# Optimization experiments

Measured on AMD Instinct MI355X. Metric: run time of the kernel, lower is better.

The kernel has to match this reference:

```python
import jax, jax.numpy as jnp
import numpy as np

TREE = 128
BASIC = 128
EPS = 1e-5


def layer_norm(x, g, b):
    m = jnp.mean(x, axis=-1, keepdims=True)
    v = jnp.mean((x - m) ** 2, axis=-1, keepdims=True)
    return (x - m) * jax.lax.rsqrt(v + EPS) * g + b


def setup_inputs() -> dict:
    key = jax.random.key(0)
    ks = jax.random.split(key, 32)
    n2, n1, n0 = 320000, 80000, 20000
    inp = {
        'subtree_h_top': jax.random.normal(ks[0], (n2, TREE), jnp.float32),
        'atom_x_1': jax.random.normal(ks[1], (n1, BASIC), jnp.float32),
        'atom_x_0': jax.random.normal(ks[2], (n0, BASIC), jnp.float32),
        'bond_x_2': jax.random.normal(ks[3], (n2, BASIC), jnp.float32),
        'bond_x_1': jax.random.normal(ks[4], (n1, BASIC), jnp.float32),
        'branch_W1': jax.random.normal(ks[5], (2, TREE + BASIC, TREE), jnp.float32) * 0.05,
        'branch_b1': jnp.zeros((2, TREE), jnp.float32),
        'branch_g1': jnp.ones((2, TREE), jnp.float32),
        'branch_beta1': jnp.zeros((2, TREE), jnp.float32),
        'branch_W2': jax.random.normal(ks[6], (2, TREE, TREE), jnp.float32) * 0.05,
        'branch_b2': jnp.zeros((2, TREE), jnp.float32),
        'branch_g2': jnp.ones((2, TREE), jnp.float32),
        'branch_beta2': jnp.zeros((2, TREE), jnp.float32),
        'sub_W1': jax.random.normal(ks[7], (2, BASIC + TREE, TREE), jnp.float32) * 0.05,
        'sub_b1': jnp.zeros((2, TREE), jnp.float32),
        'sub_g1': jnp.ones((2, TREE), jnp.float32),
        'sub_beta1': jnp.zeros((2, TREE), jnp.float32),
        'sub_W2': jax.random.normal(ks[8], (2, TREE, TREE), jnp.float32) * 0.05,
        'sub_b2': jnp.zeros((2, TREE), jnp.float32),
        'sub_g2': jnp.ones((2, TREE), jnp.float32),
        'sub_beta2': jnp.zeros((2, TREE), jnp.float32),
        'head_W': jax.random.normal(ks[9], (2, BASIC + TREE, TREE), jnp.float32) * 0.05,
        'head_b': jnp.zeros((2, TREE), jnp.float32),
        'head_g': jnp.ones((2, TREE), jnp.float32),
        'head_beta': jnp.zeros((2, TREE), jnp.float32),
        'src_2': jax.random.randint(ks[10], (n2,), 0, n2),
        'dst_2': jax.random.randint(ks[11], (n2,), 0, n1),
        'src_1': jax.random.randint(ks[12], (n1,), 0, n1),
        'dst_1': jax.random.randint(ks[13], (n1,), 0, n0),
    }
    return inp


def reference(subtree_h_top, atom_x_1, atom_x_0, bond_x_2, bond_x_1,
              branch_W1, branch_b1, branch_g1, branch_beta1,
              branch_W2, branch_b2, branch_g2, branch_beta2,
              sub_W1, sub_b1, sub_g1, sub_beta1,
              sub_W2, sub_b2, sub_g2, sub_beta2,
              head_W, head_b, head_g, head_beta,
              src_2, dst_2, src_1, dst_1):
    relu = jax.nn.relu
    h = subtree_h_top  # subtree_h of level tree_level nodes
    atom_xs = (atom_x_1, atom_x_0)
    bond_xs = (bond_x_2, bond_x_1)
    srcs = (src_2, src_1)
    dsts = (dst_2, dst_1)
    for i in range(2):  # i=0 -> k=2, i=1 -> k=1 (fixed small loop over tree levels)
        ax = atom_xs[i]
        # Branch_Update: edge MLP on [subtree_h[src], bond_x]
        ex = jnp.concatenate([h[srcs[i]], bond_xs[i]], axis=-1)  # [E, tree+basic]
        bh = relu(layer_norm(ex @ branch_W1[i] + branch_b1[i], branch_g1[i], branch_beta1[i]))
        bh = relu(layer_norm(bh @ branch_W2[i] + branch_b2[i], branch_g2[i], branch_beta2[i]))
        # fn.sum aggregation per destination (head) node
        agg = jax.ops.segment_sum(bh, dsts[i], num_segments=ax.shape[0])
        # Tree_Update_Sep
        sx = jnp.concatenate([ax, agg], axis=-1)  # [N, basic+tree]
        f = relu(layer_norm(sx @ sub_W1[i] + sub_b1[i], sub_g1[i], sub_beta1[i]))
        f = relu(layer_norm(f @ sub_W2[i] + sub_b2[i], sub_g2[i], sub_beta2[i]))
        th = jnp.concatenate([ax, f], axis=-1)
        h = relu(layer_norm(th @ head_W[i] + head_b[i], head_g[i], head_beta[i]))
    return h  # subtree_h of atom_0 nodes: [n0, tree_dim]
```

## Files before the change

kernel.cpp:

```cpp
#include <hip/hip_runtime.h>


#define D    128
#define TE   64
#define XS   264
#define TE2  32
#define MAXT 40

typedef float  f32x4 __attribute__((ext_vector_type(4)));
typedef _Float16 f16x8 __attribute__((ext_vector_type(8)));

__device__ __forceinline__ unsigned short f2h(float f) {
    union { _Float16 h; unsigned short u; } x;
    x.h = (_Float16)f;
    return x.u;
}

__global__ __launch_bounds__(256) void pack_zero(
    const float* __restrict__ brW1, const float* __restrict__ brW2,
    const float* __restrict__ sW1,  const float* __restrict__ sW2,
    const float* __restrict__ hW,   unsigned short* __restrict__ Wp,
    int* __restrict__ cnt, int AN)
{
    int p = blockIdx.x * 256 + threadIdx.x;
    if (p < AN) cnt[p] = 0;
    const float* src; int off, K;
    if (p < 65536)       { src = brW1; off = 0;      K = 256; }
    else if (p < 98304)  { src = brW2; off = 65536;  K = 128; }
    else if (p < 163840) { src = sW1;  off = 98304;  K = 256; }
    else if (p < 196608) { src = sW2;  off = 163840; K = 128; }
    else                 { src = hW;   off = 196608; K = 256; }
    int q = p - off, lvl, r;
    if (K == 256) { lvl = q >> 15; r = q & 32767; }
    else          { lvl = q >> 14; r = q & 16383; }
    int kb = r >> 12, n = (r >> 5) & 127, kk = r & 31;
    Wp[p] = f2h(src[(size_t)lvl * K * 128 + (size_t)(kb * 32 + kk) * 128 + n]);
}


__global__ __launch_bounds__(256) void csr_hist(
    const int* __restrict__ dA, int EA, const int* __restrict__ dB, int EB,
    int* __restrict__ cnt, int AOFFv)
{
    int i = blockIdx.x * 256 + threadIdx.x;
    if (i < EA)               atomicAdd(cnt + dA[i], 1);
    else if (i - EA < EB)     atomicAdd(cnt + AOFFv + dB[i - EA], 1);
}

__global__ __launch_bounds__(256) void csr_scanA(
    const int* __restrict__ cnt, int* __restrict__ inc, int* __restrict__ bsum,
    int nbA, int AOFFv)
{
    __shared__ int lds[256];
    int b = blockIdx.x, t = threadIdx.x;
    int lb, ebase, bs;
    if (b < nbA) { lb = b;       ebase = 0;     bs = lb; }
    else         { lb = b - nbA; ebase = AOFFv; bs = 128 + lb; }
    int idx = ebase + lb * 1024 + t * 4;
    int s0 = cnt[idx], s1 = cnt[idx + 1], s2 = cnt[idx + 2], s3 = cnt[idx + 3];
    int p1 = s0 + s1, p2 = p1 + s2, p3 = p2 + s3;
    lds[t] = p3; __syncthreads();
#pragma unroll
    for (int o = 1; o < 256; o <<= 1) {
        int v = (t >= o) ? lds[t - o] : 0;
        __syncthreads();
        lds[t] += v;
        __syncthreads();
    }
    int ex = lds[t] - p3;
    inc[idx] = ex + s0; inc[idx + 1] = ex + p1; inc[idx + 2] = ex + p2; inc[idx + 3] = ex + p3;
    if (t == 255) bsum[bs] = lds[255];
}

__global__ __launch_bounds__(256) void csr_scanC2(
    const int* __restrict__ cnt, int* __restrict__ inc, const int* __restrict__ bsum,
    int* __restrict__ cursor, int nbA, int nbB, int AOFFv)
{
    __shared__ int lds[256];
    int b = blockIdx.x, t = threadIdx.x;
    int seg = t >> 7, i = t & 127;
    int n = seg ? nbB : nbA;
    lds[t] = (i < n) ? bsum[t] : 0;
    __syncthreads();
#pragma unroll
    for (int o = 1; o < 128; o <<= 1) {
        int v = (i >= o) ? lds[t - o] : 0;
        __syncthreads();
        lds[t] += v;
        __syncthreads();
    }
    int lb, ebase, bs;
    if (b < nbA) { lb = b;       ebase = 0;     bs = lb; }
    else         { lb = b - nbA; ebase = AOFFv; bs = 128 + lb; }
    int carry = (lb > 0) ? lds[bs - 1] : 0;
    int idx = ebase + lb * 1024 + t * 4;
#pragma unroll
    for (int j = 0; j < 4; ++j) {
        int v = inc[idx + j] + carry;
        inc[idx + j] = v;
        cursor[idx + j] = v - cnt[idx + j];
    }
}

__global__ __launch_bounds__(256) void csr_pos(
    const int* __restrict__ dA, int EA, const int* __restrict__ dB, int EB,
    int* __restrict__ cursor, int* __restrict__ posA, int* __restrict__ posB, int AOFFv)
{
    int i = blockIdx.x * 256 + threadIdx.x;
    if (i < EA)           posA[i] = atomicAdd(cursor + dA[i], 1);
    else if (i - EA < EB) posB[i - EA] = atomicAdd(cursor + AOFFv + dB[i - EA], 1);
}


__device__ __forceinline__ void ln_relu32(f32x4 acc[4],
    const float* __restrict__ b, const float* __restrict__ g, const float* __restrict__ be,
    float* s_red, float* s_ms, int rb, int cb, int n15, int q, int wcol, int t)
{
#pragma unroll
    for (int ct = 0; ct < 4; ++ct) {
        float bb = b[cb + ct * 16 + n15];
#pragma unroll
        for (int r = 0; r < 4; ++r) acc[ct][r] += bb;
    }
    float sum[4], ss[4];
#pragma unroll
    for (int r = 0; r < 4; ++r) {
        sum[r] = acc[0][r] + acc[1][r] + acc[2][r] + acc[3][r];
        ss[r]  = acc[0][r]*acc[0][r] + acc[1][r]*acc[1][r]
               + acc[2][r]*acc[2][r] + acc[3][r]*acc[3][r];
    }
#pragma unroll
    for (int off = 1; off < 16; off <<= 1) {
#pragma unroll
        for (int r = 0; r < 4; ++r) {
            sum[r] += __shfl_xor(sum[r], off, 64);
            ss[r]  += __shfl_xor(ss[r],  off, 64);
        }
    }
    if (n15 == 0) {
#pragma unroll
        for (int r = 0; r < 4; ++r) {
            int row = rb + q * 4 + r;
            s_red[row * 4 + wcol * 2 + 0] = sum[r];
            s_red[row * 4 + wcol * 2 + 1] = ss[r];
        }
    }
    __syncthreads();
    if (t < TE2) {
        float sm = s_red[t * 4 + 0] + s_red[t * 4 + 2];
        float sq = s_red[t * 4 + 1] + s_red[t * 4 + 3];
        float mean = sm * (1.f / 128.f);
        float var  = sq * (1.f / 128.f) - mean * mean;
        s_ms[t * 2 + 0] = mean;
        s_ms[t * 2 + 1] = rsqrtf(var + 1e-5f);
    }
    __syncthreads();
#pragma unroll
    for (int ct = 0; ct < 4; ++ct) {
        float gg = g[cb + ct * 16 + n15], bb = be[cb + ct * 16 + n15];
#pragma unroll
        for (int r = 0; r < 4; ++r) {
            int row = rb + q * 4 + r;
            float v = (acc[ct][r] - s_ms[row * 2 + 0]) * s_ms[row * 2 + 1] * gg + bb;
            acc[ct][r] = fmaxf(v, 0.f);
        }
    }
}

template<bool HBF16>
__global__ __launch_bounds__(256, 1) void edge_async(
    const void* __restrict__ hsrc, const float* __restrict__ bond,
    const int* __restrict__ src, const int* __restrict__ dstpos,
    const unsigned short* __restrict__ Wp1g, const unsigned short* __restrict__ Wp2g,
    const float* __restrict__ b1, const float* __restrict__ g1, const float* __restrict__ be1,
    const float* __restrict__ b2, const float* __restrict__ g2, const float* __restrict__ be2,
    unsigned short* __restrict__ ebh, int E, int ntiles, int chunk)
{
    __shared__ unsigned short s_w1[32768];
    __shared__ unsigned short s_w2[16384];
    __shared__ unsigned short s_x[2][8192];
    __shared__ int   s_meta[MAXT * 64];
    __shared__ float s_red[TE2 * 4];
    __shared__ float s_ms[TE2 * 2];

    int t = threadIdx.x;
    int tile0 = blockIdx.x * chunk;
    int myT = ntiles - tile0;
    if (myT > chunk) myT = chunk;

    {
        const uint4* w1 = (const uint4*)Wp1g;
        for (int u = t; u < 4096; u += 256) {
            int kb = u >> 9, l = u & 511, n = l >> 2;
            *(uint4*)((char*)s_w1 + kb * 8192 + ((l ^ ((n >> 1) & 3)) << 4)) = w1[u];
        }
        const uint4* w2 = (const uint4*)Wp2g;
        for (int u = t; u < 2048; u += 256) {
            int kb = u >> 9, l = u & 511, n = l >> 2;
            *(uint4*)((char*)s_w2 + kb * 8192 + ((l ^ ((n >> 1) & 3)) << 4)) = w2[u];
        }
        for (int x = t; x < myT * 64; x += 256) {
            int ti = x >> 6, r = x & 63;
            int ge = (tile0 + ti) * TE2 + (r & 31);
            int v;
            if (r < 32) v = (ge < E) ? src[ge] : 0;
            else        v = (ge < E) ? dstpos[ge] : -1;
            s_meta[x] = v;
        }
    }
    __syncthreads();
    if (myT <= 0) return;

    int r0  = t >> 5, k4 = t & 31;
    int r0h = t >> 4, k8 = t & 15;

    {
        if (HBF16) {
            const unsigned short* hp = (const unsigned short*)hsrc;
#pragma unroll
            for (int j = 0; j < 2; ++j) {
                int row = r0h + 16 * j;
                int sv = s_meta[row];
                uint4 v = *(const uint4*)(hp + (size_t)sv * 128 + k8 * 8);
                *(uint4*)((char*)&s_x[0][0] + row * 512 + ((k8 ^ (row & 7)) << 4)) = v;
            }
        } else {
            const float* hp = (const float*)hsrc;
#pragma unroll
            for (int j = 0; j < 4; ++j) {
                int row = r0 + 8 * j;
                int sv = s_meta[row];
                float4 v = *(const float4*)(hp + (size_t)sv * 128 + k4 * 4);
                ushort4 o; o.x = f2h(v.x); o.y = f2h(v.y); o.z = f2h(v.z); o.w = f2h(v.w);
                *(ushort4*)((char*)&s_x[0][0] + row * 512
                            + (((k4 >> 1) ^ (row & 7)) << 4) + (k4 & 1) * 8) = o;
            }
        }
#pragma unroll
        for (int j = 0; j < 4; ++j) {
            int row = r0 + 8 * j;
            int ge = tile0 * TE2 + row;
            float4 v = make_float4(0, 0, 0, 0);
            if (ge < E) v = *(const float4*)(bond + (size_t)ge * 128 + k4 * 4);
            ushort4 o; o.x = f2h(v.x); o.y = f2h(v.y); o.z = f2h(v.z); o.w = f2h(v.w);
            *(ushort4*)((char*)&s_x[0][0] + row * 512
                        + (((16 + (k4 >> 1)) ^ (row & 7)) << 4) + (k4 & 1) * 8) = o;
        }
    }
    __syncthreads();

    int lane = t & 63, w = t >> 6;
    int n15 = lane & 15, q = lane >> 4;
    int rb = (w & 1) * 16, cb = (w >> 1) * 64, wcol = w >> 1;

    int c = 0;
    for (int i = 0; i < myT; ++i) {
        bool hasN = (i + 1 < myT);
        uint4  nh16[2]; float4 nh32[4]; float4 nb[4];
        if (hasN) {
            int mt = i + 1, tb = (tile0 + mt) * TE2;
            if (HBF16) {
                const unsigned short* hp = (const unsigned short*)hsrc;
#pragma unroll
                for (int j = 0; j < 2; ++j) {
                    int row = r0h + 16 * j;
                    int sv = s_meta[mt * 64 + row];
                    nh16[j] = *(const uint4*)(hp + (size_t)sv * 128 + k8 * 8);
                }
            } else {
                const float* hp = (const float*)hsrc;
#pragma unroll
                for (int j = 0; j < 4; ++j) {
                    int row = r0 + 8 * j;
                    int sv = s_meta[mt * 64 + row];
                    nh32[j] = *(const float4*)(hp + (size_t)sv * 128 + k4 * 4);
                }
            }
#pragma unroll
            for (int j = 0; j < 4; ++j) {
                int row = r0 + 8 * j, ge = tb + row;
                nb[j] = make_float4(0, 0, 0, 0);
                if (ge < E) nb[j] = *(const float4*)(bond + (size_t)ge * 128 + k4 * 4);
            }
        }

        const unsigned short* xb = &s_x[c][0];
        unsigned short* f1b = (unsigned short*)&s_x[c ^ 1][0];
        unsigned short* f2b = f1b + 4096;

        f32x4 acc[4];
        f32x4 zero = {0.f, 0.f, 0.f, 0.f};
#pragma unroll
        for (int ct = 0; ct < 4; ++ct) acc[ct] = zero;
#pragma unroll
        for (int kb = 0; kb < 8; ++kb) {
            f16x8 af = *(const f16x8*)((const char*)xb + (rb + n15) * 512
                                       + (((kb * 4 + q) ^ (n15 & 7)) << 4));
#pragma unroll
            for (int ct = 0; ct < 4; ++ct) {
                int n = cb + ct * 16 + n15, l = n * 4 + q;
                f16x8 bf = *(const f16x8*)((const char*)s_w1 + kb * 8192
                                           + ((l ^ ((n >> 1) & 3)) << 4));
                acc[ct] = __builtin_amdgcn_mfma_f32_16x16x32_f16(af, bf, acc[ct], 0, 0, 0);
            }
        }
        ln_relu32(acc, b1, g1, be1, s_red, s_ms, rb, cb, n15, q, wcol, t);
#pragma unroll
        for (int ct = 0; ct < 4; ++ct)
#pragma unroll
            for (int r = 0; r < 4; ++r) {
                int row = rb + q * 4 + r, col = cb + ct * 16 + n15;
                *(unsigned short*)((char*)f1b + row * 256
                                   + ((col * 2) ^ ((row & 7) << 4))) = f2h(acc[ct][r]);
            }
        __syncthreads();

#pragma unroll
        for (int ct = 0; ct < 4; ++ct) acc[ct] = zero;
#pragma unroll
        for (int kb = 0; kb < 4; ++kb) {
            f16x8 af = *(const f16x8*)((const char*)f1b + (rb + n15) * 256
                                       + (((kb * 4 + q) ^ (n15 & 7)) << 4));
#pragma unroll
            for (int ct = 0; ct < 4; ++ct) {
                int n = cb + ct * 16 + n15, l = n * 4 + q;
                f16x8 bf = *(const f16x8*)((const char*)s_w2 + kb * 8192
                                           + ((l ^ ((n >> 1) & 3)) << 4));
                acc[ct] = __builtin_amdgcn_mfma_f32_16x16x32_f16(af, bf, acc[ct], 0, 0, 0);
            }
        }
        ln_relu32(acc, b2, g2, be2, s_red, s_ms, rb, cb, n15, q, wcol, t);
#pragma unroll
        for (int ct = 0; ct < 4; ++ct)
#pragma unroll
            for (int r = 0; r < 4; ++r) {
                int row = rb + q * 4 + r, col = cb + ct * 16 + n15;
                *(unsigned short*)((char*)f2b + row * 256
                                   + ((col * 2) ^ ((row & 7) << 4))) = f2h(acc[ct][r]);
            }
        __syncthreads();

#pragma unroll
        for (int j = 0; j < 2; ++j) {
            int row = r0h + 16 * j;
            int p = s_meta[i * 64 + 32 + row];
            if (p >= 0) {
                uint4 v = *(const uint4*)((const char*)f2b + row * 256
                                          + ((k8 ^ (row & 7)) << 4));
                *(uint4*)(ebh + (size_t)p * 128 + k8 * 8) = v;
            }
        }
        __syncthreads();

        if (hasN) {
            unsigned short* dstb = (unsigned short*)&s_x[c ^ 1][0];
            if (HBF16) {
#pragma unroll
                for (int j = 0; j < 2; ++j) {
                    int row = r0h + 16 * j;
                    *(uint4*)((char*)dstb + row * 512 + ((k8 ^ (row & 7)) << 4)) = nh16[j];
                }
            } else {
#pragma unroll
                for (int j = 0; j < 4; ++j) {
                    int row = r0 + 8 * j;
                    ushort4 o;
                    o.x = f2h(nh32[j].x); o.y = f2h(nh32[j].y);
                    o.z = f2h(nh32[j].z); o.w = f2h(nh32[j].w);
                    *(ushort4*)((char*)dstb + row * 512
                                + (((k4 >> 1) ^ (row & 7)) << 4) + (k4 & 1) * 8) = o;
                }
            }
#pragma unroll
            for (int j = 0; j < 4; ++j) {
                int row = r0 + 8 * j;
                ushort4 o;
                o.x = f2h(nb[j].x); o.y = f2h(nb[j].y); o.z = f2h(nb[j].z); o.w = f2h(nb[j].w);
                *(ushort4*)((char*)dstb + row * 512
                            + (((16 + (k4 >> 1)) ^ (row & 7)) << 4) + (k4 & 1) * 8) = o;
            }
        }
        __syncthreads();
        c ^= 1;
    }
}


template<int KB>
__device__ __forceinline__ void gemm_f16(const unsigned short* s_in, int stride,
    const unsigned short* __restrict__ Wp, int rb, int cb, int n15, int q, f32x4 acc[2][4])
{
    f32x4 zero = {0.f, 0.f, 0.f, 0.f};
#pragma unroll
    for (int m = 0; m < 2; ++m)
#pragma unroll
        for (int ct = 0; ct < 4; ++ct) acc[m][ct] = zero;
#pragma unroll
    for (int kb = 0; kb < KB; ++kb) {
        f16x8 af0 = *(const f16x8*)(s_in + (rb + n15) * stride + kb * 32 + q * 8);
        f16x8 af1 = *(const f16x8*)(s_in + (rb + 16 + n15) * stride + kb * 32 + q * 8);
        const unsigned short* wb = Wp + (size_t)kb * 4096 + q * 8;
#pragma unroll
        for (int ct = 0; ct < 4; ++ct) {
            f16x8 bf = *(const f16x8*)(wb + (cb + ct * 16 + n15) * 32);
            acc[0][ct] = __builtin_amdgcn_mfma_f32_16x16x32_f16(af0, bf, acc[0][ct], 0, 0, 0);
            acc[1][ct] = __builtin_amdgcn_mfma_f32_16x16x32_f16(af1, bf, acc[1][ct], 0, 0, 0);
        }
    }
}

__device__ __forceinline__ void ln_relu(f32x4 acc[2][4],
    const float* __restrict__ b, const float* __restrict__ g, const float* __restrict__ be,
    float* s_red, float* s_ms, int rb, int cb, int n15, int q, int wcol, int t)
{
#pragma unroll
    for (int ct = 0; ct < 4; ++ct) {
        float bb = b[cb + ct * 16 + n15];
#pragma unroll
        for (int m = 0; m < 2; ++m)
#pragma unroll
            for (int r = 0; r < 4; ++r) acc[m][ct][r] += bb;
    }
    float sum[2][4], ss[2][4];
#pragma unroll
    for (int m = 0; m < 2; ++m)
#pragma unroll
        for (int r = 0; r < 4; ++r) {
            sum[m][r] = acc[m][0][r] + acc[m][1][r] + acc[m][2][r] + acc[m][3][r];
            ss[m][r]  = acc[m][0][r]*acc[m][0][r] + acc[m][1][r]*acc[m][1][r]
                      + acc[m][2][r]*acc[m][2][r] + acc[m][3][r]*acc[m][3][r];
        }
#pragma unroll
    for (int off = 1; off < 16; off <<= 1) {
#pragma unroll
        for (int m = 0; m < 2; ++m)
#pragma unroll
            for (int r = 0; r < 4; ++r) {
                sum[m][r] += __shfl_xor(sum[m][r], off, 64);
                ss[m][r]  += __shfl_xor(ss[m][r],  off, 64);
            }
    }
    if (n15 == 0) {
#pragma unroll
        for (int m = 0; m < 2; ++m)
#pragma unroll
            for (int r = 0; r < 4; ++r) {
                int row = rb + m * 16 + q * 4 + r;
                s_red[row * 4 + wcol * 2 + 0] = sum[m][r];
                s_red[row * 4 + wcol * 2 + 1] = ss[m][r];
            }
    }
    __syncthreads();
    if (t < TE) {
        float sm = s_red[t * 4 + 0] + s_red[t * 4 + 2];
        float sq = s_red[t * 4 + 1] + s_red[t * 4 + 3];
        float mean = sm * (1.f / 128.f);
        float var  = sq * (1.f / 128.f) - mean * mean;
        s_ms[t * 2 + 0] = mean;
        s_ms[t * 2 + 1] = rsqrtf(var + 1e-5f);
    }
    __syncthreads();
#pragma unroll
    for (int ct = 0; ct < 4; ++ct) {
        float gg = g[cb + ct * 16 + n15], bb = be[cb + ct * 16 + n15];
#pragma unroll
        for (int m = 0; m < 2; ++m)
#pragma unroll
            for (int r = 0; r < 4; ++r) {
                int row = rb + m * 16 + q * 4 + r;
                float v = (acc[m][ct][r] - s_ms[row * 2 + 0]) * s_ms[row * 2 + 1] * gg + bb;
                acc[m][ct][r] = fmaxf(v, 0.f);
            }
    }
}

template<bool HBF16, bool CSR>
__global__ __launch_bounds__(256, 4) void edge_mlp(
    const void* __restrict__ hsrc, const float* __restrict__ bond,
    const int* __restrict__ src, const int* __restrict__ dstpos,
    const unsigned short* __restrict__ Wp1, const unsigned short* __restrict__ Wp2,
    const float* __restrict__ b1, const float* __restrict__ g1, const float* __restrict__ be1,
    const float* __restrict__ b2, const float* __restrict__ g2, const float* __restrict__ be2,
    float* __restrict__ agg, unsigned short* __restrict__ ebh, int E)
{
    __shared__ unsigned short s_x[TE * XS];
    __shared__ float s_red[TE * 4];
    __shared__ float s_ms[TE * 2];
    __shared__ int s_src[TE], s_idx[TE];
    unsigned short* s_y = s_x + 128;

    int t = threadIdx.x, eb = blockIdx.x * TE;
    if (t < TE) {
        int ge = eb + t;
        s_src[t] = (ge < E) ? src[ge] : -1;
        s_idx[t] = (ge < E) ? dstpos[ge] : -1;
    }
    __syncthreads();

    if (HBF16) {
        const unsigned short* hp = (const unsigned short*)hsrc;
        for (int c = t; c < TE * 16; c += 256) {
            int row = c >> 4, k8 = c & 15;
            int s = s_src[row];
            uint4 v = make_uint4(0, 0, 0, 0);
            if (s >= 0) v = *(const uint4*)(hp + (size_t)s * 128 + k8 * 8);
            *(uint4*)(s_x + row * XS + k8 * 8) = v;
        }
    } else {
        const float* hp = (const float*)hsrc;
        for (int c = t; c < TE * 32; c += 256) {
            int row = c >> 5, k4 = c & 31;
            int s = s_src[row];
            float4 v = make_float4(0, 0, 0, 0);
            if (s >= 0) v = *(const float4*)(hp + (size_t)s * 128 + k4 * 4);
            ushort4 o; o.x = f2h(v.x); o.y = f2h(v.y); o.z = f2h(v.z); o.w = f2h(v.w);
            *(ushort4*)(s_x + row * XS + k4 * 4) = o;
        }
    }
    for (int c = t; c < TE * 32; c += 256) {
        int row = c >> 5, k4 = c & 31;
        int ge = eb + row;
        float4 v = make_float4(0, 0, 0, 0);
        if (ge < E) v = *(const float4*)(bond + (size_t)ge * 128 + k4 * 4);
        ushort4 o; o.x = f2h(v.x); o.y = f2h(v.y); o.z = f2h(v.z); o.w = f2h(v.w);
        *(ushort4*)(s_x + row * XS + 128 + k4 * 4) = o;
    }
    __syncthreads();

    int l = t & 63, w = t >> 6;
    int n15 = l & 15, q = l >> 4;
    int rb = (w & 1) * 32, cb = (w >> 1) * 64, wcol = w >> 1;

    f32x4 acc[2][4];
    gemm_f16<8>(s_x, XS, Wp1, rb, cb, n15, q, acc);
    ln_relu(acc, b1, g1, be1, s_red, s_ms, rb, cb, n15, q, wcol, t);
#pragma unroll
    for (int m = 0; m < 2; ++m)
#pragma unroll
        for (int ct = 0; ct < 4; ++ct)
#pragma unroll
            for (int r = 0; r < 4; ++r)
                s_y[(rb + m * 16 + q * 4 + r) * XS + cb + ct * 16 + n15] = f2h(acc[m][ct][r]);
    __syncthreads();
    gemm_f16<4>(s_y, XS, Wp2, rb, cb, n15, q, acc);
    ln_relu(acc, b2, g2, be2, s_red, s_ms, rb, cb, n15, q, wcol, t);

    if (CSR) {
#pragma unroll
        for (int m = 0; m < 2; ++m)
#pragma unroll
            for (int ct = 0; ct < 4; ++ct)
#pragma unroll
                for (int r = 0; r < 4; ++r)
                    s_x[(rb + m * 16 + q * 4 + r) * XS + cb + ct * 16 + n15] = f2h(acc[m][ct][r]);
        __syncthreads();
        for (int c = t; c < TE * 16; c += 256) {
            int row = c >> 4, k8 = c & 15;
            int p = s_idx[row];
            if (p >= 0)
                *(uint4*)(ebh + (size_t)p * 128 + k8 * 8) =
                    *(const uint4*)(s_x + row * XS + k8 * 8);
        }
    } else {
#pragma unroll
        for (int m = 0; m < 2; ++m)
#pragma unroll
            for (int ct = 0; ct < 4; ++ct)
#pragma unroll
                for (int r = 0; r < 4; ++r) {
                    int row = rb + m * 16 + q * 4 + r;
                    int gd = s_idx[row];
                    if (gd >= 0)
                        atomicAdd(agg + (size_t)gd * D + cb + ct * 16 + n15, acc[m][ct][r]);
                }
    }
}

template<bool OUT_F16, bool CSR>
__global__ __launch_bounds__(256, 4) void node_mlp(
    const float* __restrict__ ax, const float* __restrict__ agg,
    const int* __restrict__ inc, const unsigned short* __restrict__ ebh,
    const unsigned short* __restrict__ Wp1, const unsigned short* __restrict__ Wp2,
    const unsigned short* __restrict__ Wp3,
    const float* __restrict__ b1, const float* __restrict__ g1, const float* __restrict__ be1,
    const float* __restrict__ b2, const float* __restrict__ g2, const float* __restrict__ be2,
    const float* __restrict__ b3, const float* __restrict__ g3, const float* __restrict__ be3,
    void* __restrict__ out, int N)
{
    __shared__ unsigned short s_x[TE * XS];
    __shared__ float s_red[TE * 4];
    __shared__ float s_ms[TE * 2];
    __shared__ int s_beg[TE], s_end[TE];
    unsigned short* s_y = s_x + 128;

    int t = threadIdx.x, nb = blockIdx.x * TE;

    if (CSR && t < TE) {
        int gr = nb + t, b0 = 0, e0 = 0;
        if (gr < N) { e0 = inc[gr]; b0 = (gr == 0) ? 0 : inc[gr - 1]; }
        s_beg[t] = b0; s_end[t] = e0;
    }

    for (int c = t; c < TE * 32; c += 256) {
        int row = c >> 5, k4 = c & 31;
        int gr = nb + row;
        float4 v = make_float4(0, 0, 0, 0);
        if (gr < N) v = *(const float4*)(ax + (size_t)gr * 128 + k4 * 4);
        ushort4 o; o.x = f2h(v.x); o.y = f2h(v.y); o.z = f2h(v.z); o.w = f2h(v.w);
        *(ushort4*)(s_x + row * XS + k4 * 4) = o;
    }

    if (CSR) {
        __syncthreads();
        int r = t >> 2, s4 = t & 3;
        float a[32];
#pragma unroll
        for (int k = 0; k < 32; ++k) a[k] = 0.f;
        int jb = s_beg[r], je = s_end[r];
        int j = jb;
        for (; j + 2 <= je; j += 2) {
            const unsigned short* rp0 = ebh + (size_t)j * 128 + s4 * 32;
            const unsigned short* rp1 = rp0 + 128;
            f16x8 a0 = *(const f16x8*)rp0;
            f16x8 a1 = *(const f16x8*)(rp0 + 8);
            f16x8 a2 = *(const f16x8*)(rp0 + 16);
            f16x8 a3 = *(const f16x8*)(rp0 + 24);
            f16x8 b0 = *(const f16x8*)rp1;
            f16x8 b1v = *(const f16x8*)(rp1 + 8);
            f16x8 b2v = *(const f16x8*)(rp1 + 16);
            f16x8 b3v = *(const f16x8*)(rp1 + 24);
#pragma unroll
            for (int k = 0; k < 8; ++k) {
                a[k]      += (float)a0[k];
                a[8 + k]  += (float)a1[k];
                a[16 + k] += (float)a2[k];
                a[24 + k] += (float)a3[k];
            }
#pragma unroll
            for (int k = 0; k < 8; ++k) {
                a[k]      += (float)b0[k];
                a[8 + k]  += (float)b1v[k];
                a[16 + k] += (float)b2v[k];
                a[24 + k] += (float)b3v[k];
            }
        }
        if (j < je) {
            const unsigned short* rp = ebh + (size_t)j * 128 + s4 * 32;
            f16x8 v0 = *(const f16x8*)rp;
            f16x8 v1 = *(const f16x8*)(rp + 8);
            f16x8 v2 = *(const f16x8*)(rp + 16);
            f16x8 v3 = *(const f16x8*)(rp + 24);
#pragma unroll
            for (int k = 0; k < 8; ++k) {
                a[k]      += (float)v0[k];
                a[8 + k]  += (float)v1[k];
                a[16 + k] += (float)v2[k];
                a[24 + k] += (float)v3[k];
            }
        }
        unsigned short* op = s_x + r * XS + 128 + s4 * 32;
#pragma unroll
        for (int blk = 0; blk < 4; ++blk) {
            f16x8 h;
#pragma unroll
            for (int k = 0; k < 8; ++k) h[k] = (_Float16)a[blk * 8 + k];
            *(f16x8*)(op + blk * 8) = h;
        }
    } else {
        for (int c = t; c < TE * 32; c += 256) {
            int row = c >> 5, k4 = c & 31;
            int gr = nb + row;
            float4 v = make_float4(0, 0, 0, 0);
            if (gr < N) v = *(const float4*)(agg + (size_t)gr * 128 + k4 * 4);
            ushort4 o; o.x = f2h(v.x); o.y = f2h(v.y); o.z = f2h(v.z); o.w = f2h(v.w);
            *(ushort4*)(s_x + row * XS + 128 + k4 * 4) = o;
        }
    }
    __syncthreads();

    int l = t & 63, w = t >> 6;
    int n15 = l & 15, q = l >> 4;
    int rb = (w & 1) * 32, cb = (w >> 1) * 64, wcol = w >> 1;

    f32x4 acc[2][4];
    gemm_f16<8>(s_x, XS, Wp1, rb, cb, n15, q, acc);
    ln_relu(acc, b1, g1, be1, s_red, s_ms, rb, cb, n15, q, wcol, t);
#pragma unroll
    for (int m = 0; m < 2; ++m)
#pragma unroll
        for (int ct = 0; ct < 4; ++ct)
#pragma unroll
            for (int r = 0; r < 4; ++r)
                s_y[(rb + m * 16 + q * 4 + r) * XS + cb + ct * 16 + n15] = f2h(acc[m][ct][r]);
    __syncthreads();
    gemm_f16<4>(s_y, XS, Wp2, rb, cb, n15, q, acc);
    ln_relu(acc, b2, g2, be2, s_red, s_ms, rb, cb, n15, q, wcol, t);
#pragma unroll
    for (int m = 0; m < 2; ++m)
#pragma unroll
        for (int ct = 0; ct < 4; ++ct)
#pragma unroll
            for (int r = 0; r < 4; ++r)
                s_x[(rb + m * 16 + q * 4 + r) * XS + 128 + cb + ct * 16 + n15] = f2h(acc[m][ct][r]);
    __syncthreads();
    gemm_f16<8>(s_x, XS, Wp3, rb, cb, n15, q, acc);
    ln_relu(acc, b3, g3, be3, s_red, s_ms, rb, cb, n15, q, wcol, t);

#pragma unroll
    for (int m = 0; m < 2; ++m)
#pragma unroll
        for (int ct = 0; ct < 4; ++ct)
#pragma unroll
            for (int r = 0; r < 4; ++r) {
                int row = rb + m * 16 + q * 4 + r;
                int gr = nb + row;
                int col = cb + ct * 16 + n15;
                if (gr < N) {
                    if (OUT_F16)
                        ((unsigned short*)out)[(size_t)gr * D + col] = f2h(acc[m][ct][r]);
                    else
                        ((float*)out)[(size_t)gr * D + col] = acc[m][ct][r];
                }
            }
}

extern "C" void kernel_launch(void* const* d_in, const int* in_sizes, int n_in,
                              void* d_out, int out_size, void* d_ws, size_t ws_size,
                              hipStream_t stream)
{
    const float* h2   = (const float*)d_in[0];
    const float* ax1  = (const float*)d_in[1];
    const float* ax0  = (const float*)d_in[2];
    const float* bx2  = (const float*)d_in[3];
    const float* bx1  = (const float*)d_in[4];
    const float* brW1 = (const float*)d_in[5];
    const float* brb1 = (const float*)d_in[6];
    const float* brg1 = (const float*)d_in[7];
    const float* brbe1= (const float*)d_in[8];
    const float* brW2 = (const float*)d_in[9];
    const float* brb2 = (const float*)d_in[10];
    const float* brg2 = (const float*)d_in[11];
    const float* brbe2= (const float*)d_in[12];
    const float* sW1  = (const float*)d_in[13];
    const float* sb1  = (const float*)d_in[14];
    const float* sg1  = (const float*)d_in[15];
    const float* sbe1 = (const float*)d_in[16];
    const float* sW2  = (const float*)d_in[17];
    const float* sb2  = (const float*)d_in[18];
    const float* sg2  = (const float*)d_in[19];
    const float* sbe2 = (const float*)d_in[20];
    const float* hW   = (const float*)d_in[21];
    const float* hb   = (const float*)d_in[22];
    const float* hg   = (const float*)d_in[23];
    const float* hbe  = (const float*)d_in[24];
    const int*   src2 = (const int*)d_in[25];
    const int*   dst2 = (const int*)d_in[26];
    const int*   src1 = (const int*)d_in[27];
    const int*   dst1 = (const int*)d_in[28];

    int n2 = in_sizes[0] / D;
    int n1 = in_sizes[1] / D;
    int n0 = in_sizes[2] / D;

    unsigned short* Wp = (unsigned short*)d_ws;

    const unsigned short* pBr1[2] = { Wp + 0,      Wp + 32768 };
    const unsigned short* pBr2[2] = { Wp + 65536,  Wp + 65536  + 16384 };
    const unsigned short* pS1 [2] = { Wp + 98304,  Wp + 98304  + 32768 };
    const unsigned short* pS2 [2] = { Wp + 163840, Wp + 163840 + 16384 };
    const unsigned short* pH  [2] = { Wp + 196608, Wp + 196608 + 32768 };

    int nbA = (n1 + 1023) / 1024, nbB = (n0 + 1023) / 1024;
    int AOFFv = nbA * 1024;
    int AN = AOFFv + nbB * 1024;
    auto al = [](size_t x) { return (x + 255) & ~(size_t)255; };
    size_t o = 524288;
    size_t cnt_o  = o; o = al(o + (size_t)AN * 4);
    size_t inc_o  = o; o = al(o + (size_t)AN * 4);
    size_t cur_o  = o; o = al(o + (size_t)AN * 4);
    size_t bsum_o = o; o = al(o + 1024);
    size_t posA_o = o; o = al(o + (size_t)n2 * 4);
    size_t posB_o = o; o = al(o + (size_t)n1 * 4);
    size_t h1_o   = o; o = al(o + (size_t)n1 * 256);
    size_t ebh_o  = o; o = al(o + (size_t)n2 * 256);
    size_t o_csr  = o;
    bool use_csr = (nbA <= 128) && (nbB <= 128) && (ws_size >= o_csr);

    int t2e = (n2 + TE - 1) / TE, t1e = (n1 + TE - 1) / TE;
    int t1n = (n1 + TE - 1) / TE, t0n = (n0 + TE - 1) / TE;

    if (use_csr) {
        int*            cnt    = (int*)((char*)d_ws + cnt_o);
        int*            inc    = (int*)((char*)d_ws + inc_o);
        int*            cursor = (int*)((char*)d_ws + cur_o);
        int*            bsum   = (int*)((char*)d_ws + bsum_o);
        int*            posA   = (int*)((char*)d_ws + posA_o);
        int*            posB   = (int*)((char*)d_ws + posB_o);
        unsigned short* h1     = (unsigned short*)((char*)d_ws + h1_o);
        unsigned short* ebh    = (unsigned short*)((char*)d_ws + ebh_o);

        int EG = (n2 + n1 + 255) / 256;
        pack_zero<<<dim3(1024), dim3(256), 0, stream>>>(brW1, brW2, sW1, sW2, hW, Wp, cnt, AN);
        csr_hist  <<<dim3(EG),        dim3(256), 0, stream>>>(dst2, n2, dst1, n1, cnt, AOFFv);
        csr_scanA <<<dim3(nbA + nbB), dim3(256), 0, stream>>>(cnt, inc, bsum, nbA, AOFFv);
        csr_scanC2<<<dim3(nbA + nbB), dim3(256), 0, stream>>>(cnt, inc, bsum, cursor, nbA, nbB, AOFFv);
        csr_pos   <<<dim3(EG),        dim3(256), 0, stream>>>(dst2, n2, dst1, n1, cursor, posA, posB, AOFFv);

        int tiles2 = (n2 + TE2 - 1) / TE2, chunk2 = (tiles2 + 255) / 256;
        bool asy2 = (chunk2 <= MAXT);

        if (asy2)
            edge_async<false><<<dim3(256), dim3(256), 0, stream>>>(
                h2, bx2, src2, posA, pBr1[0], pBr2[0],
                brb1, brg1, brbe1, brb2, brg2, brbe2, ebh, n2, tiles2, chunk2);
        else
            edge_mlp<false, true><<<dim3(t2e), dim3(256), 0, stream>>>(
                h2, bx2, src2, posA, pBr1[0], pBr2[0],
                brb1, brg1, brbe1, brb2, brg2, brbe2, nullptr, ebh, n2);
        node_mlp<true, true><<<dim3(t1n), dim3(256), 0, stream>>>(
            ax1, nullptr, inc, ebh, pS1[0], pS2[0], pH[0],
            sb1, sg1, sbe1, sb2, sg2, sbe2, hb, hg, hbe, h1, n1);

        edge_mlp<true, true><<<dim3(t1e), dim3(256), 0, stream>>>(
            h1, bx1, src1, posB, pBr1[1], pBr2[1],
            brb1 + D, brg1 + D, brbe1 + D, brb2 + D, brg2 + D, brbe2 + D, nullptr, ebh, n1);
        node_mlp<false, true><<<dim3(t0n), dim3(256), 0, stream>>>(
            ax0, nullptr, inc + AOFFv, ebh, pS1[1], pS2[1], pH[1],
            sb1 + D, sg1 + D, sbe1 + D, sb2 + D, sg2 + D, sbe2 + D,
            hb + D, hg + D, hbe + D, d_out, n0);
    } else {
        float*          agg = (float*)((char*)d_ws + 524288);
        unsigned short* h1  = (unsigned short*)(agg + (size_t)n1 * D);

        pack_zero<<<dim3(1024), dim3(256), 0, stream>>>(brW1, brW2, sW1, sW2, hW, Wp, nullptr, 0);

        hipMemsetAsync(agg, 0, (size_t)n1 * D * sizeof(float), stream);
        edge_mlp<false, false><<<dim3(t2e), dim3(256), 0, stream>>>(
            h2, bx2, src2, dst2, pBr1[0], pBr2[0],
            brb1, brg1, brbe1, brb2, brg2, brbe2, agg, nullptr, n2);
        node_mlp<true, false><<<dim3(t1n), dim3(256), 0, stream>>>(
            ax1, agg, nullptr, nullptr, pS1[0], pS2[0], pH[0],
            sb1, sg1, sbe1, sb2, sg2, sbe2, hb, hg, hbe, h1, n1);

        hipMemsetAsync(agg, 0, (size_t)n0 * D * sizeof(float), stream);
        edge_mlp<true, false><<<dim3(t1e), dim3(256), 0, stream>>>(
            h1, bx1, src1, dst1, pBr1[1], pBr2[1],
            brb1 + D, brg1 + D, brbe1 + D, brb2 + D, brg2 + D, brbe2 + D, agg, nullptr, n1);
        node_mlp<false, false><<<dim3(t0n), dim3(256), 0, stream>>>(
            ax0, agg, nullptr, nullptr, pS1[1], pS2[1], pH[1],
            sb1 + D, sg1 + D, sbe1 + D, sb2 + D, sg2 + D, sbe2 + D,
            hb + D, hg + D, hbe + D, d_out, n0);
    }
}
```

Before: 656.5 us.

## Add persistent node_async kernel for level-1 node MLP with resident weights

Adds a persistent kernel for the level-1 node update. It runs 256 blocks, each looping over a contiguous chunk of 32-row tiles. Sub-MLP weights are loaded once into LDS and kept resident, and the next tile's atom features are prefetched into a double buffer while the current tile computes. This is meant to remove the repeated per-tile weight loads and launch granularity of the old node_mlp. In exchange it uses one block per CU, and the head weights are read from global memory each tile.

Measured after the change: 700.9 us. 6.8% more time.

```diff
diff --git a/kernel.cpp b/kernel.cpp
--- a/kernel.cpp
+++ b/kernel.cpp
@@ -167,6 +167,7 @@
     }
 }
 
+
 template<bool HBF16>
 __global__ __launch_bounds__(256, 1) void edge_async(
     const void* __restrict__ hsrc, const float* __restrict__ bond,
@@ -378,6 +379,243 @@
                 o.x = f2h(nb[j].x); o.y = f2h(nb[j].y); o.z = f2h(nb[j].z); o.w = f2h(nb[j].w);
                 *(ushort4*)((char*)dstb + row * 512
                             + (((16 + (k4 >> 1)) ^ (row & 7)) << 4) + (k4 & 1) * 8) = o;
+            }
+        }
+        __syncthreads();
+        c ^= 1;
+    }
+}
+
+__global__ __launch_bounds__(256, 1) void node_async(
+    const float* __restrict__ ax,
+    const int* __restrict__ inc, const unsigned short* __restrict__ ebh,
+    const unsigned short* __restrict__ Wp1g, const unsigned short* __restrict__ Wp2g,
+    const unsigned short* __restrict__ Wp3,
+    const float* __restrict__ b1, const float* __restrict__ g1, const float* __restrict__ be1,
+    const float* __restrict__ b2, const float* __restrict__ g2, const float* __restrict__ be2,
+    const float* __restrict__ b3, const float* __restrict__ g3, const float* __restrict__ be3,
+    unsigned short* __restrict__ out, int N, int ntiles, int chunk)
+{
+    __shared__ unsigned short s_w1[32768];
+    __shared__ unsigned short s_w2[16384];
+    __shared__ unsigned short s_x[2][8192];
+    __shared__ int   s_meta[MAXT * 64];
+    __shared__ float s_red[TE2 * 4];
+    __shared__ float s_ms[TE2 * 2];
+
+    int t = threadIdx.x;
+    int tile0 = blockIdx.x * chunk;
+    int myT = ntiles - tile0;
+    if (myT > chunk) myT = chunk;
+
+    {
+        const uint4* w1 = (const uint4*)Wp1g;
+        for (int u = t; u < 4096; u += 256) {
+            int kb = u >> 9, l = u & 511, n = l >> 2;
+            *(uint4*)((char*)s_w1 + kb * 8192 + ((l ^ ((n >> 1) & 3)) << 4)) = w1[u];
+        }
+        const uint4* w2 = (const uint4*)Wp2g;
+        for (int u = t; u < 2048; u += 256) {
+            int kb = u >> 9, l = u & 511, n = l >> 2;
+            *(uint4*)((char*)s_w2 + kb * 8192 + ((l ^ ((n >> 1) & 3)) << 4)) = w2[u];
+        }
+        for (int x = t; x < myT * 64; x += 256) {
+            int ti = x >> 6, r = x & 63;
+            int gr = (tile0 + ti) * TE2 + (r & 31);
+            int v = 0;
+            if (gr < N) {
+                if (r < 32) v = (gr == 0) ? 0 : inc[gr - 1];
+                else        v = inc[gr];
+            }
+            s_meta[x] = v;
+        }
+    }
+    __syncthreads();
+    if (myT <= 0) return;
+
+    int r0  = t >> 5, k4 = t & 31;
+    int r0h = t >> 4, k8 = t & 15;
+
+    {
+#pragma unroll
+        for (int j = 0; j < 4; ++j) {
+            int row = r0 + 8 * j;
+            int gr = tile0 * TE2 + row;
+            float4 v = make_float4(0, 0, 0, 0);
+            if (gr < N) v = *(const float4*)(ax + (size_t)gr * 128 + k4 * 4);
+            ushort4 o; o.x = f2h(v.x); o.y = f2h(v.y); o.z = f2h(v.z); o.w = f2h(v.w);
+            *(ushort4*)((char*)&s_x[0][0] + row * 512
+                        + (((k4 >> 1) ^ (row & 7)) << 4) + (k4 & 1) * 8) = o;
+        }
+    }
+    __syncthreads();
+
+    int lane = t & 63, w = t >> 6;
+    int n15 = lane & 15, q = lane >> 4;
+    int rb = (w & 1) * 16, cb = (w >> 1) * 64, wcol = w >> 1;
+    int sr = t >> 3, s8 = t & 7;
+
+    int c = 0;
+    for (int i = 0; i < myT; ++i) {
+        unsigned short* xb = (unsigned short*)&s_x[c][0];
+        unsigned short* f1b = (unsigned short*)&s_x[c ^ 1][0];
+        unsigned short* f2b = f1b + 4096;
+
+        {
+            int jb = s_meta[i * 64 + sr], je = s_meta[i * 64 + 32 + sr];
+            float a[16];
+#pragma unroll
+            for (int k = 0; k < 16; ++k) a[k] = 0.f;
+            int j = jb;
+            for (; j + 2 <= je; j += 2) {
+                const unsigned short* rp0 = ebh + (size_t)j * 128 + s8 * 16;
+                const unsigned short* rp1 = rp0 + 128;
+                f16x8 v0 = *(const f16x8*)rp0;
+                f16x8 v1 = *(const f16x8*)(rp0 + 8);
+                f16x8 u0 = *(const f16x8*)rp1;
+                f16x8 u1 = *(const f16x8*)(rp1 + 8);
+#pragma unroll
+                for (int k = 0; k < 8; ++k) { a[k] += (float)v0[k]; a[8 + k] += (float)v1[k]; }
+#pragma unroll
+                for (int k = 0; k < 8; ++k) { a[k] += (float)u0[k]; a[8 + k] += (float)u1[k]; }
+            }
+            if (j < je) {
+                const unsigned short* rp = ebh + (size_t)j * 128 + s8 * 16;
+                f16x8 v0 = *(const f16x8*)rp;
+                f16x8 v1 = *(const f16x8*)(rp + 8);
+#pragma unroll
+                for (int k = 0; k < 8; ++k) { a[k] += (float)v0[k]; a[8 + k] += (float)v1[k]; }
+            }
+            f16x8 h0, h1;
+#pragma unroll
+            for (int k = 0; k < 8; ++k) { h0[k] = (_Float16)a[k]; h1[k] = (_Float16)a[8 + k]; }
+            int u0i = 16 + 2 * s8, u1i = u0i + 1;
+            *(f16x8*)((char*)xb + sr * 512 + ((u0i ^ (sr & 7)) << 4)) = h0;
+            *(f16x8*)((char*)xb + sr * 512 + ((u1i ^ (sr & 7)) << 4)) = h1;
+        }
+        __syncthreads();
+
+        bool hasN = (i + 1 < myT);
+        float4 nax[4];
+        if (hasN) {
+            int tb = (tile0 + i + 1) * TE2;
+#pragma unroll
+            for (int j = 0; j < 4; ++j) {
+                int row = r0 + 8 * j, gr = tb + row;
+                nax[j] = make_float4(0, 0, 0, 0);
+                if (gr < N) nax[j] = *(const float4*)(ax + (size_t)gr * 128 + k4 * 4);
+            }
+        }
+
+        f32x4 acc[4];
+        f32x4 zero = {0.f, 0.f, 0.f, 0.f};
+#pragma unroll
+        for (int ct = 0; ct < 4; ++ct) acc[ct] = zero;
+#pragma unroll
+        for (int kb = 0; kb < 8; ++kb) {
+            f16x8 af = *(const f16x8*)((const char*)xb + (rb + n15) * 512
+                                       + (((kb * 4 + q) ^ (n15 & 7)) << 4));
+#pragma unroll
+            for (int ct = 0; ct < 4; ++ct) {
+                int n = cb + ct * 16 + n15, l = n * 4 + q;
+                f16x8 bf = *(const f16x8*)((const char*)s_w1 + kb * 8192
+                                           + ((l ^ ((n >> 1) & 3)) << 4));
+                acc[ct] = __builtin_amdgcn_mfma_f32_16x16x32_f16(af, bf, acc[ct], 0, 0, 0);
+            }
+        }
+        ln_relu32(acc, b1, g1, be1, s_red, s_ms, rb, cb, n15, q, wcol, t);
+#pragma unroll
+        for (int ct = 0; ct < 4; ++ct)
+#pragma unroll
+            for (int r = 0; r < 4; ++r) {
+                int row = rb + q * 4 + r, col = cb + ct * 16 + n15;
+                *(unsigned short*)((char*)f1b + row * 256
+                                   + ((col * 2) ^ ((row & 7) << 4))) = f2h(acc[ct][r]);
+            }
+        __syncthreads();
+
+#pragma unroll
+        for (int ct = 0; ct < 4; ++ct) acc[ct] = zero;
+#pragma unroll
+        for (int kb = 0; kb < 4; ++kb) {
+            f16x8 af = *(const f16x8*)((const char*)f1b + (rb + n15) * 256
+                                       + (((kb * 4 + q) ^ (n15 & 7)) << 4));
+#pragma unroll
+            for (int ct = 0; ct < 4; ++ct) {
+                int n = cb + ct * 16 + n15, l = n * 4 + q;
+                f16x8 bf = *(const f16x8*)((const char*)s_w2 + kb * 8192
+                                           + ((l ^ ((n >> 1) & 3)) << 4));
+                acc[ct] = __builtin_amdgcn_mfma_f32_16x16x32_f16(af, bf, acc[ct], 0, 0, 0);
+            }
+        }
+        ln_relu32(acc, b2, g2, be2, s_red, s_ms, rb, cb, n15, q, wcol, t);
+#pragma unroll
+        for (int ct = 0; ct < 4; ++ct)
+#pragma unroll
+            for (int r = 0; r < 4; ++r) {
+                int row = rb + q * 4 + r, col = cb + ct * 16 + n15;
+                *(unsigned short*)((char*)f2b + row * 256
+                                   + ((col * 2) ^ ((row & 7) << 4))) = f2h(acc[ct][r]);
+            }
+        __syncthreads();
+
+#pragma unroll
+        for (int ct = 0; ct < 4; ++ct) acc[ct] = zero;
+#pragma unroll
+        for (int kb = 0; kb < 4; ++kb) {
+            f16x8 af = *(const f16x8*)((const char*)xb + (rb + n15) * 512
+                                       + (((kb * 4 + q) ^ (n15 & 7)) << 4));
+            const unsigned short* wb = Wp3 + (size_t)kb * 4096 + q * 8;
+#pragma unroll
+            for (int ct = 0; ct < 4; ++ct) {
+                f16x8 bf = *(const f16x8*)(wb + (cb + ct * 16 + n15) * 32);
+                acc[ct] = __builtin_amdgcn_mfma_f32_16x16x32_f16(af, bf, acc[ct], 0, 0, 0);
+            }
+        }
+#pragma unroll
+        for (int kb = 0; kb < 4; ++kb) {
+            f16x8 af = *(const f16x8*)((const char*)f2b + (rb + n15) * 256
+                                       + (((kb * 4 + q) ^ (n15 & 7)) << 4));
+            const unsigned short* wb = Wp3 + (size_t)(kb + 4) * 4096 + q * 8;
+#pragma unroll
+            for (int ct = 0; ct < 4; ++ct) {
+                f16x8 bf = *(const f16x8*)(wb + (cb + ct * 16 + n15) * 32);
+                acc[ct] = __builtin_amdgcn_mfma_f32_16x16x32_f16(af, bf, acc[ct], 0, 0, 0);
+            }
+        }
+        ln_relu32(acc, b3, g3, be3, s_red, s_ms, rb, cb, n15, q, wcol, t);
+
+#pragma unroll
+        for (int ct = 0; ct < 4; ++ct)
+#pragma unroll
+            for (int r = 0; r < 4; ++r) {
+                int row = rb + q * 4 + r, col = cb + ct * 16 + n15;
+                *(unsigned short*)((char*)f1b + row * 256
+                                   + ((col * 2) ^ ((row & 7) << 4))) = f2h(acc[ct][r]);
+            }
+        __syncthreads();
+#pragma unroll
+        for (int j = 0; j < 2; ++j) {
+            int row = r0h + 16 * j;
+            int gr = (tile0 + i) * TE2 + row;
+            if (gr < N) {
+                uint4 v = *(const uint4*)((const char*)f1b + row * 256
+                                          + ((k8 ^ (row & 7)) << 4));
+                *(uint4*)(out + (size_t)gr * 128 + k8 * 8) = v;
+            }
+        }
+        __syncthreads();
+
+        if (hasN) {
+            unsigned short* dstb = (unsigned short*)&s_x[c ^ 1][0];
+#pragma unroll
+            for (int j = 0; j < 4; ++j) {
+                int row = r0 + 8 * j;
+                ushort4 o;
+                o.x = f2h(nax[j].x); o.y = f2h(nax[j].y);
+                o.z = f2h(nax[j].z); o.w = f2h(nax[j].w);
+                *(ushort4*)((char*)dstb + row * 512
+                            + (((k4 >> 1) ^ (row & 7)) << 4) + (k4 & 1) * 8) = o;
             }
         }
         __syncthreads();
@@ -808,6 +1046,8 @@
 
         int tiles2 = (n2 + TE2 - 1) / TE2, chunk2 = (tiles2 + 255) / 256;
         bool asy2 = (chunk2 <= MAXT);
+        int tiles1n = (n1 + TE2 - 1) / TE2, chunk1n = (tiles1n + 255) / 256;
+        bool asyn1 = (chunk1n <= MAXT);
 
         if (asy2)
             edge_async<false><<<dim3(256), dim3(256), 0, stream>>>(
@@ -817,9 +1057,14 @@
             edge_mlp<false, true><<<dim3(t2e), dim3(256), 0, stream>>>(
                 h2, bx2, src2, posA, pBr1[0], pBr2[0],
                 brb1, brg1, brbe1, brb2, brg2, brbe2, nullptr, ebh, n2);
-        node_mlp<true, true><<<dim3(t1n), dim3(256), 0, stream>>>(
-            ax1, nullptr, inc, ebh, pS1[0], pS2[0], pH[0],
-            sb1, sg1, sbe1, sb2, sg2, sbe2, hb, hg, hbe, h1, n1);
+        if (asyn1)
+            node_async<<<dim3(256), dim3(256), 0, stream>>>(
+                ax1, inc, ebh, pS1[0], pS2[0], pH[0],
+                sb1, sg1, sbe1, sb2, sg2, sbe2, hb, hg, hbe, h1, n1, tiles1n, chunk1n);
+        else
+            node_mlp<true, true><<<dim3(t1n), dim3(256), 0, stream>>>(
+                ax1, nullptr, inc, ebh, pS1[0], pS2[0], pH[0],
+                sb1, sg1, sbe1, sb2, sg2, sbe2, hb, hg, hbe, h1, n1);
 
         edge_mlp<true, true><<<dim3(t1e), dim3(256), 0, stream>>>(
             h1, bx1, src1, posB, pBr1[1], pBr2[1],
```
